# Performance work log

Measured on AMD Instinct MI355X. Metric: run time of the kernel, lower is better.

## Reference

```python
import jax, jax.numpy as jnp
import numpy as np

N_NODES = 50000
N_EDGES = 800000
IN_CH, HID_CH, OUT_CH = 128, 128, 64


def setup_inputs() -> dict:
    key = jax.random.key(0)
    k1, k2, k3, k4, k5, k6 = jax.random.split(key, 6)
    x = jax.random.normal(k1, (N_NODES, IN_CH), dtype=jnp.float32)
    edge_index = jax.random.randint(k2, (2, N_EDGES), 0, N_NODES, dtype=jnp.int64)
    # Glorot init like PyG GCNConv; bias zeros-like but random small for test coverage
    s1 = jnp.sqrt(6.0 / (IN_CH + HID_CH)).astype(jnp.float32)
    s2 = jnp.sqrt(6.0 / (HID_CH + OUT_CH)).astype(jnp.float32)
    W1 = jax.random.uniform(k3, (IN_CH, HID_CH), jnp.float32, -s1, s1)
    b1 = jax.random.normal(k4, (HID_CH,), jnp.float32) * 0.01
    W2 = jax.random.uniform(k5, (HID_CH, OUT_CH), jnp.float32, -s2, s2)
    b2 = jax.random.normal(k6, (OUT_CH,), jnp.float32) * 0.01
    return {"x": x, "edge_index": edge_index, "W1": W1, "b1": b1, "W2": W2, "b2": b2}


def gcn_conv(x, edge_index, W, b):
    """PyG GCNConv: add self-loops, symmetric D^-1/2 (A+I) D^-1/2 normalization,
    then aggregate linearly-transformed neighbor features + bias."""
    n = x.shape[0]
    h = x @ W  # [N, F_out]
    src, dst = edge_index[0], edge_index[1]
    # degree counts self-loop (weight 1) plus in-edges at dst
    deg = 1.0 + jax.ops.segment_sum(jnp.ones_like(src, dtype=h.dtype), dst, num_segments=n)
    dinv = jax.lax.rsqrt(deg)  # deg >= 1, no zeros
    norm = dinv[src] * dinv[dst]  # [E]
    agg = jax.ops.segment_sum(h[src] * norm[:, None], dst, num_segments=n)
    # self-loop contribution: norm = dinv[i]*dinv[i] = 1/deg[i]
    return agg + h * (1.0 / deg)[:, None] + b


def reference(x, edge_index, W1, b1, W2, b2):
    # eval-mode forward: dropout is identity
    h = gcn_conv(x, edge_index, W1, b1)
    h = jax.nn.relu(h)
    out = gcn_conv(h, edge_index, W2, b2)
    return out
```

## Files before the change

### kernel.cpp

```cpp
#include <hip/hip_runtime.h>
#include <hip/hip_fp16.h>


typedef _Float16 f16;
typedef __attribute__((ext_vector_type(8))) _Float16 f16x8;
typedef __attribute__((ext_vector_type(4))) float f32x4;

__global__ __launch_bounds__(256) void deg_prep_kernel(const int* __restrict__ dst,
                                                       int* __restrict__ deg,
                                                       int* __restrict__ posw,
                                                       const float* __restrict__ W1,
                                                       const float* __restrict__ W2,
                                                       f16* __restrict__ Wt1,
                                                       f16* __restrict__ Wt2, int E) {
    int gid = blockIdx.x * 256 + threadIdx.x;
    if (gid < E) posw[gid] = atomicAdd(&deg[dst[gid]], 1);
    if (gid < 128 * 128) {
        int k = gid >> 7, c = gid & 127;
        Wt1[c * 136 + k] = (f16)W1[gid];
    } else if (gid < 128 * 128 + 128 * 64) {
        int j = gid - 128 * 128;
        int k = j >> 6, c = j & 63;
        Wt2[c * 136 + k] = (f16)W2[j];
    }
}

__global__ __launch_bounds__(1024) void scan1_kernel(const int* __restrict__ deg,
                                                     int* __restrict__ rowptr,
                                                     int* __restrict__ bsum,
                                                     float* __restrict__ dinv, int N) {
    __shared__ int wsum[16];
    const int tid = threadIdx.x, lane = tid & 63, wid = tid >> 6;
    const int idx = blockIdx.x * 1024 + tid;
    int v = (idx < N) ? deg[idx] : 0;
    if (idx < N) dinv[idx] = rsqrtf((float)v + 1.0f);
    int incl = v;
#pragma unroll
    for (int off = 1; off < 64; off <<= 1) {
        int t = __shfl_up(incl, off, 64);
        if (lane >= off) incl += t;
    }
    if (lane == 63) wsum[wid] = incl;
    __syncthreads();
    if (wid == 0) {
        int s = (lane < 16) ? wsum[lane] : 0;
#pragma unroll
        for (int off = 1; off < 16; off <<= 1) {
            int t = __shfl_up(s, off, 64);
            if (lane >= off) s += t;
        }
        if (lane < 16) wsum[lane] = s;
    }
    __syncthreads();
    int waveoff = (wid == 0) ? 0 : wsum[wid - 1];
    if (idx < N) rowptr[idx] = waveoff + incl - v;
    if (tid == 1023) bsum[blockIdx.x] = waveoff + incl;
}

__global__ __launch_bounds__(1024) void scan23_kernel(int* __restrict__ rowptr,
                                                      const int* __restrict__ bsum,
                                                      int N, int nb) {
    __shared__ int pfx_s;
    const int tid = threadIdx.x;
    if (tid < 64) {
        int v = (tid < nb && tid < blockIdx.x) ? bsum[tid] : 0;
#pragma unroll
        for (int off = 32; off; off >>= 1) v += __shfl_xor(v, off, 64);
        if (tid == 0) pfx_s = v;
    }
    if (blockIdx.x == 0 && tid >= 64 && tid < 128) {
        int l = tid - 64;
        int v = (l < nb) ? bsum[l] : 0;
#pragma unroll
        for (int off = 32; off; off >>= 1) v += __shfl_xor(v, off, 64);
        if (l == 0) rowptr[N] = v;
    }
    __syncthreads();
    int idx = blockIdx.x * 1024 + tid;
    if (idx < N) rowptr[idx] += pfx_s;
}

__global__ __launch_bounds__(256) void fill_kernel(const int* __restrict__ src,
                                                   const int* __restrict__ dst,
                                                   const int* __restrict__ posw,
                                                   const float* __restrict__ dinv,
                                                   const int* __restrict__ rowptr,
                                                   float2* __restrict__ pairs, int E) {
    int e = blockIdx.x * 256 + threadIdx.x;
    if (e >= E) return;
    int s = src[e], d = dst[e];
    float2 p;
    p.x = __int_as_float(s);
    p.y = dinv[s] * dinv[d];
    pairs[rowptr[d] + posw[e]] = p;
}

template <int KOUT, bool F32IN>
__global__ __launch_bounds__(256) void gemm_kernel(const void* __restrict__ Xv,
                                                   const f16* __restrict__ Wt,
                                                   f16* __restrict__ H, int N) {
    constexpr int CT = KOUT / 16;
    __shared__ f16 Wl[KOUT * 136];
    const int tid = threadIdx.x;
    constexpr int CHUNKS = KOUT * 136 / 8;
    {
        const uint4* s = (const uint4*)Wt;
        uint4* d = (uint4*)Wl;
        for (int i = tid; i < CHUNKS; i += 256) d[i] = s[i];
    }
    __syncthreads();

    const int lane = tid & 63, wid = tid >> 6;
    const int c = lane & 15, kseg = lane >> 4;
    const int row0 = blockIdx.x * 64 + wid * 16;
    int arow = row0 + c;
    if (arow >= N) arow = N - 1;

    f32x4 acc[CT];
#pragma unroll
    for (int t = 0; t < CT; ++t) acc[t] = (f32x4){0.f, 0.f, 0.f, 0.f};

#pragma unroll
    for (int kt = 0; kt < 4; ++kt) {
        const int k0 = kt * 32;
        f16x8 a;
        if (F32IN) {
            const float* xp = (const float*)Xv + (long)arow * 128 + k0 + kseg * 8;
            float4 x0 = *(const float4*)xp;
            float4 x1 = *(const float4*)(xp + 4);
            a[0] = (f16)x0.x; a[1] = (f16)x0.y; a[2] = (f16)x0.z; a[3] = (f16)x0.w;
            a[4] = (f16)x1.x; a[5] = (f16)x1.y; a[6] = (f16)x1.z; a[7] = (f16)x1.w;
        } else {
            a = *(const f16x8*)((const f16*)Xv + (long)arow * 128 + k0 + kseg * 8);
        }
#pragma unroll
        for (int ct = 0; ct < CT; ++ct) {
            f16x8 b = *(const f16x8*)&Wl[(ct * 16 + c) * 136 + k0 + kseg * 8];
            acc[ct] = __builtin_amdgcn_mfma_f32_16x16x32_f16(a, b, acc[ct], 0, 0, 0);
        }
    }

    const int rbase = row0 + kseg * 4;
#pragma unroll
    for (int ct = 0; ct < CT; ++ct)
#pragma unroll
        for (int r = 0; r < 4; ++r) {
            int row = rbase + r;
            if (row < N) H[(long)row * KOUT + ct * 16 + c] = (f16)acc[ct][r];
        }
}

template <int F, bool RELU, bool OUTF16>
__global__ __launch_bounds__(256) void gather_kernel(const void* __restrict__ Hv,
                                                     const int* __restrict__ rowptr,
                                                     const float2* __restrict__ pairs,
                                                     const float* __restrict__ dinv,
                                                     const float* __restrict__ bias,
                                                     void* __restrict__ outv, int N) {
    const int wid = threadIdx.x >> 6;
    const int lane = threadIdx.x & 63;
    const int node = blockIdx.x * 4 + wid;
    if (node >= N) return;
    const int start = rowptr[node], end = rowptr[node + 1];

    if (F == 128) {
        const __half2* Hu = (const __half2*)Hv;
        float ax = 0.f, ay = 0.f;
        int e = start;
        for (; e + 7 < end; e += 8) {
            float2 pp[8];
            __half2 uu[8];
#pragma unroll
            for (int j = 0; j < 8; ++j) pp[j] = pairs[e + j];
#pragma unroll
            for (int j = 0; j < 8; ++j) uu[j] = Hu[(long)__float_as_int(pp[j].x) * 64 + lane];
#pragma unroll
            for (int j = 0; j < 8; ++j) {
                float2 f = __half22float2(uu[j]);
                ax += f.x * pp[j].y;
                ay += f.y * pp[j].y;
            }
        }
        for (; e + 3 < end; e += 4) {
            float2 pp[4];
            __half2 uu[4];
#pragma unroll
            for (int j = 0; j < 4; ++j) pp[j] = pairs[e + j];
#pragma unroll
            for (int j = 0; j < 4; ++j) uu[j] = Hu[(long)__float_as_int(pp[j].x) * 64 + lane];
#pragma unroll
            for (int j = 0; j < 4; ++j) {
                float2 f = __half22float2(uu[j]);
                ax += f.x * pp[j].y;
                ay += f.y * pp[j].y;
            }
        }
        for (; e < end; ++e) {
            float2 p0 = pairs[e];
            float2 f0 = __half22float2(Hu[(long)__float_as_int(p0.x) * 64 + lane]);
            ax += f0.x * p0.y;
            ay += f0.y * p0.y;
        }
        float di = dinv[node];
        float d2 = di * di;
        float2 fs = __half22float2(Hu[(long)node * 64 + lane]);
        float2 bz = ((const float2*)bias)[lane];
        float zx = ax + fs.x * d2 + bz.x;
        float zy = ay + fs.y * d2 + bz.y;
        if (RELU) { zx = fmaxf(zx, 0.f); zy = fmaxf(zy, 0.f); }
        if (OUTF16) {
            ((__half2*)outv)[(long)node * 64 + lane] = __float22half2_rn(make_float2(zx, zy));
        } else {
            float2 o = {zx, zy};
            ((float2*)outv)[(long)node * 64 + lane] = o;
        }
    } else {
        const __half* Hh = (const __half*)Hv;
        float acc = 0.f;
        int e = start;
        for (; e + 7 < end; e += 8) {
            float2 pp[8];
            __half uu[8];
#pragma unroll
            for (int j = 0; j < 8; ++j) pp[j] = pairs[e + j];
#pragma unroll
            for (int j = 0; j < 8; ++j) uu[j] = Hh[(long)__float_as_int(pp[j].x) * 64 + lane];
#pragma unroll
            for (int j = 0; j < 8; ++j) acc += __half2float(uu[j]) * pp[j].y;
        }
        for (; e + 3 < end; e += 4) {
            float2 pp[4];
            __half uu[4];
#pragma unroll
            for (int j = 0; j < 4; ++j) pp[j] = pairs[e + j];
#pragma unroll
            for (int j = 0; j < 4; ++j) uu[j] = Hh[(long)__float_as_int(pp[j].x) * 64 + lane];
#pragma unroll
            for (int j = 0; j < 4; ++j) acc += __half2float(uu[j]) * pp[j].y;
        }
        for (; e < end; ++e) {
            float2 p0 = pairs[e];
            acc += __half2float(Hh[(long)__float_as_int(p0.x) * 64 + lane]) * p0.y;
        }
        float di = dinv[node];
        float z = acc + __half2float(Hh[(long)node * 64 + lane]) * (di * di) + bias[lane];
        if (RELU) z = fmaxf(z, 0.f);
        ((float*)outv)[(long)node * 64 + lane] = z;
    }
}

extern "C" void kernel_launch(void* const* d_in, const int* in_sizes, int n_in,
                              void* d_out, int out_size, void* d_ws, size_t ws_size,
                              hipStream_t stream) {
    const float* x  = (const float*)d_in[0];
    const int*   ei = (const int*)d_in[1];
    const float* W1 = (const float*)d_in[2];
    const float* b1 = (const float*)d_in[3];
    const float* W2 = (const float*)d_in[4];
    const float* b2 = (const float*)d_in[5];
    float* out = (float*)d_out;

    const int N = in_sizes[0] / 128;
    const int E = in_sizes[1] / 2;
    const int* src = ei;
    const int* dst = ei + E;
    const int NB = (N + 1023) / 1024;

    float* ws = (float*)d_ws;
    float2* pairs = (float2*)ws;
    long off = 2L * E;
    int* posw   = (int*)(ws + off); off += E;
    int* deg    = (int*)(ws + off); off += N;
    int* rowptr = (int*)(ws + off); off += N + 1;
    int* bsum   = (int*)(ws + off); off += 64;
    float* dinv = ws + off;        off += N;
    off = (off + 3) & ~3L;
    f16* Wt1 = (f16*)(ws + off); off += (128 * 136) / 2;
    f16* Wt2 = (f16*)(ws + off); off += (64 * 136) / 2;
    f16* h1  = (f16*)(ws + off); off += (long)N * 64;
    f16* z1  = (f16*)(ws + off); off += (long)N * 64;
    f16* h2  = (f16*)(ws + off); off += (long)N * 32;

    hipMemsetAsync(deg, 0, (size_t)N * sizeof(int), stream);
    deg_prep_kernel<<<(E + 255) / 256, 256, 0, stream>>>(dst, deg, posw, W1, W2, Wt1, Wt2, E);
    scan1_kernel<<<NB, 1024, 0, stream>>>(deg, rowptr, bsum, dinv, N);
    scan23_kernel<<<NB, 1024, 0, stream>>>(rowptr, bsum, N, NB);
    fill_kernel<<<(E + 255) / 256, 256, 0, stream>>>(src, dst, posw, dinv, rowptr, pairs, E);

    gemm_kernel<128, true><<<(N + 63) / 64, 256, 0, stream>>>(x, Wt1, h1, N);
    gather_kernel<128, true, true><<<(N + 3) / 4, 256, 0, stream>>>(h1, rowptr, pairs, dinv, b1, z1, N);

    gemm_kernel<64, false><<<(N + 63) / 64, 256, 0, stream>>>(z1, Wt2, h2, N);
    gather_kernel<64, false, false><<<(N + 3) / 4, 256, 0, stream>>>(h2, rowptr, pairs, dinv, b2, out, N);
}
```

Before: 228.2 us.

## Fuse CSR fill with first GEMM and vectorize gather pair loads

Merges the edge-pair fill kernel and the first-layer GEMM into one launch, with block ranges split between the two independent jobs so they run concurrently and one launch is saved. The gather kernels now read the (src, norm) pairs as float4 (two edges per load) after aligning to an even index, and unroll 16 edges per iteration for more outstanding loads. The fill blocks now reserve the 34KB shared array they do not use, which may reduce their occupancy, and the larger unroll raises register pressure.

```diff
diff --git a/kernel.cpp b/kernel.cpp
--- a/kernel.cpp
+++ b/kernel.cpp
@@ -80,27 +80,11 @@
     if (idx < N) rowptr[idx] += pfx_s;
 }
 
-__global__ __launch_bounds__(256) void fill_kernel(const int* __restrict__ src,
-                                                   const int* __restrict__ dst,
-                                                   const int* __restrict__ posw,
-                                                   const float* __restrict__ dinv,
-                                                   const int* __restrict__ rowptr,
-                                                   float2* __restrict__ pairs, int E) {
-    int e = blockIdx.x * 256 + threadIdx.x;
-    if (e >= E) return;
-    int s = src[e], d = dst[e];
-    float2 p;
-    p.x = __int_as_float(s);
-    p.y = dinv[s] * dinv[d];
-    pairs[rowptr[d] + posw[e]] = p;
-}
-
 template <int KOUT, bool F32IN>
-__global__ __launch_bounds__(256) void gemm_kernel(const void* __restrict__ Xv,
-                                                   const f16* __restrict__ Wt,
-                                                   f16* __restrict__ H, int N) {
+__device__ __forceinline__ void gemm_body(int bid, const void* __restrict__ Xv,
+                                          const f16* __restrict__ Wt,
+                                          f16* __restrict__ H, int N, f16* Wl) {
     constexpr int CT = KOUT / 16;
-    __shared__ f16 Wl[KOUT * 136];
     const int tid = threadIdx.x;
     constexpr int CHUNKS = KOUT * 136 / 8;
     {
@@ -112,7 +96,7 @@
 
     const int lane = tid & 63, wid = tid >> 6;
     const int c = lane & 15, kseg = lane >> 4;
-    const int row0 = blockIdx.x * 64 + wid * 16;
+    const int row0 = bid * 64 + wid * 16;
     int arow = row0 + c;
     if (arow >= N) arow = N - 1;
 
@@ -148,6 +132,37 @@
             int row = rbase + r;
             if (row < N) H[(long)row * KOUT + ct * 16 + c] = (f16)acc[ct][r];
         }
+}
+
+template <int KOUT, bool F32IN>
+__global__ __launch_bounds__(256) void gemm_kernel(const void* __restrict__ Xv,
+                                                   const f16* __restrict__ Wt,
+                                                   f16* __restrict__ H, int N) {
+    __shared__ f16 Wl[KOUT * 136];
+    gemm_body<KOUT, F32IN>(blockIdx.x, Xv, Wt, H, N, Wl);
+}
+
+__global__ __launch_bounds__(256) void fill_gemm_kernel(const int* __restrict__ src,
+                                                        const int* __restrict__ dst,
+                                                        const int* __restrict__ posw,
+                                                        const float* __restrict__ dinv,
+                                                        const int* __restrict__ rowptr,
+                                                        float2* __restrict__ pairs, int E,
+                                                        const float* __restrict__ x,
+                                                        const f16* __restrict__ Wt1,
+                                                        f16* __restrict__ h1, int N, int GB) {
+    __shared__ f16 Wl[128 * 136];
+    if ((int)blockIdx.x < GB) {
+        gemm_body<128, true>(blockIdx.x, x, Wt1, h1, N, Wl);
+        return;
+    }
+    int e = (blockIdx.x - GB) * 256 + threadIdx.x;
+    if (e >= E) return;
+    int s = src[e], d = dst[e];
+    float2 p;
+    p.x = __int_as_float(s);
+    p.y = dinv[s] * dinv[d];
+    pairs[rowptr[d] + posw[e]] = p;
 }
 
 template <int F, bool RELU, bool OUTF16>
@@ -162,44 +177,51 @@
     const int node = blockIdx.x * 4 + wid;
     if (node >= N) return;
     const int start = rowptr[node], end = rowptr[node + 1];
+    const float4* pp4 = (const float4*)pairs;
 
     if (F == 128) {
         const __half2* Hu = (const __half2*)Hv;
         float ax = 0.f, ay = 0.f;
         int e = start;
-        for (; e + 7 < end; e += 8) {
-            float2 pp[8];
-            __half2 uu[8];
-#pragma unroll
-            for (int j = 0; j < 8; ++j) pp[j] = pairs[e + j];
-#pragma unroll
-            for (int j = 0; j < 8; ++j) uu[j] = Hu[(long)__float_as_int(pp[j].x) * 64 + lane];
+        if ((e & 1) && e < end) {
+            float2 p0 = pairs[e];
+            float2 f0 = __half22float2(Hu[(long)__float_as_int(p0.x) * 64 + lane]);
+            ax += f0.x * p0.y; ay += f0.y * p0.y;
+            ++e;
+        }
+        for (; e + 15 < end; e += 16) {
+            float4 q[8];
+#pragma unroll
+            for (int j = 0; j < 8; ++j) q[j] = pp4[(e >> 1) + j];
+            __half2 uu[16];
 #pragma unroll
             for (int j = 0; j < 8; ++j) {
-                float2 f = __half22float2(uu[j]);
-                ax += f.x * pp[j].y;
-                ay += f.y * pp[j].y;
+                uu[2 * j]     = Hu[(long)__float_as_int(q[j].x) * 64 + lane];
+                uu[2 * j + 1] = Hu[(long)__float_as_int(q[j].z) * 64 + lane];
             }
+#pragma unroll
+            for (int j = 0; j < 8; ++j) {
+                float2 f0 = __half22float2(uu[2 * j]);
+                float2 f1 = __half22float2(uu[2 * j + 1]);
+                ax += f0.x * q[j].y + f1.x * q[j].w;
+                ay += f0.y * q[j].y + f1.y * q[j].w;
+            }
         }
         for (; e + 3 < end; e += 4) {
-            float2 pp[4];
-            __half2 uu[4];
-#pragma unroll
-            for (int j = 0; j < 4; ++j) pp[j] = pairs[e + j];
-#pragma unroll
-            for (int j = 0; j < 4; ++j) uu[j] = Hu[(long)__float_as_int(pp[j].x) * 64 + lane];
-#pragma unroll
-            for (int j = 0; j < 4; ++j) {
-                float2 f = __half22float2(uu[j]);
-                ax += f.x * pp[j].y;
-                ay += f.y * pp[j].y;
-            }
+            float4 q0 = pp4[e >> 1], q1 = pp4[(e >> 1) + 1];
+            __half2 u0 = Hu[(long)__float_as_int(q0.x) * 64 + lane];
+            __half2 u1 = Hu[(long)__float_as_int(q0.z) * 64 + lane];
+            __half2 u2 = Hu[(long)__float_as_int(q1.x) * 64 + lane];
+            __half2 u3 = Hu[(long)__float_as_int(q1.z) * 64 + lane];
+            float2 f0 = __half22float2(u0), f1 = __half22float2(u1);
+            float2 f2 = __half22float2(u2), f3 = __half22float2(u3);
+            ax += f0.x * q0.y + f1.x * q0.w + f2.x * q1.y + f3.x * q1.w;
+            ay += f0.y * q0.y + f1.y * q0.w + f2.y * q1.y + f3.y * q1.w;
         }
         for (; e < end; ++e) {
             float2 p0 = pairs[e];
             float2 f0 = __half22float2(Hu[(long)__float_as_int(p0.x) * 64 + lane]);
-            ax += f0.x * p0.y;
-            ay += f0.y * p0.y;
+            ax += f0.x * p0.y; ay += f0.y * p0.y;
         }
         float di = dinv[node];
         float d2 = di * di;
@@ -218,25 +240,32 @@
         const __half* Hh = (const __half*)Hv;
         float acc = 0.f;
         int e = start;
-        for (; e + 7 < end; e += 8) {
-            float2 pp[8];
-            __half uu[8];
-#pragma unroll
-            for (int j = 0; j < 8; ++j) pp[j] = pairs[e + j];
-#pragma unroll
-            for (int j = 0; j < 8; ++j) uu[j] = Hh[(long)__float_as_int(pp[j].x) * 64 + lane];
-#pragma unroll
-            for (int j = 0; j < 8; ++j) acc += __half2float(uu[j]) * pp[j].y;
+        if ((e & 1) && e < end) {
+            float2 p0 = pairs[e];
+            acc += __half2float(Hh[(long)__float_as_int(p0.x) * 64 + lane]) * p0.y;
+            ++e;
+        }
+        for (; e + 15 < end; e += 16) {
+            float4 q[8];
+#pragma unroll
+            for (int j = 0; j < 8; ++j) q[j] = pp4[(e >> 1) + j];
+            __half uu[16];
+#pragma unroll
+            for (int j = 0; j < 8; ++j) {
+                uu[2 * j]     = Hh[(long)__float_as_int(q[j].x) * 64 + lane];
+                uu[2 * j + 1] = Hh[(long)__float_as_int(q[j].z) * 64 + lane];
+            }
+#pragma unroll
+            for (int j = 0; j < 8; ++j)
+                acc += __half2float(uu[2 * j]) * q[j].y + __half2float(uu[2 * j + 1]) * q[j].w;
         }
         for (; e + 3 < end; e += 4) {
-            float2 pp[4];
-            __half uu[4];
-#pragma unroll
-            for (int j = 0; j < 4; ++j) pp[j] = pairs[e + j];
-#pragma unroll
-            for (int j = 0; j < 4; ++j) uu[j] = Hh[(long)__float_as_int(pp[j].x) * 64 + lane];
-#pragma unroll
-            for (int j = 0; j < 4; ++j) acc += __half2float(uu[j]) * pp[j].y;
+            float4 q0 = pp4[e >> 1], q1 = pp4[(e >> 1) + 1];
+            float h0 = __half2float(Hh[(long)__float_as_int(q0.x) * 64 + lane]);
+            float h1 = __half2float(Hh[(long)__float_as_int(q0.z) * 64 + lane]);
+            float h2 = __half2float(Hh[(long)__float_as_int(q1.x) * 64 + lane]);
+            float h3 = __half2float(Hh[(long)__float_as_int(q1.z) * 64 + lane]);
+            acc += h0 * q0.y + h1 * q0.w + h2 * q1.y + h3 * q1.w;
         }
         for (; e < end; ++e) {
             float2 p0 = pairs[e];
@@ -285,9 +314,12 @@
     deg_prep_kernel<<<(E + 255) / 256, 256, 0, stream>>>(dst, deg, posw, W1, W2, Wt1, Wt2, E);
     scan1_kernel<<<NB, 1024, 0, stream>>>(deg, rowptr, bsum, dinv, N);
     scan23_kernel<<<NB, 1024, 0, stream>>>(rowptr, bsum, N, NB);
-    fill_kernel<<<(E + 255) / 256, 256, 0, stream>>>(src, dst, posw, dinv, rowptr, pairs, E);
-
-    gemm_kernel<128, true><<<(N + 63) / 64, 256, 0, stream>>>(x, Wt1, h1, N);
+
+    const int GB = (N + 63) / 64;
+    const int FB = (E + 255) / 256;
+    fill_gemm_kernel<<<GB + FB, 256, 0, stream>>>(src, dst, posw, dinv, rowptr, pairs, E,
+                                                  x, Wt1, h1, N, GB);
+
     gather_kernel<128, true, true><<<(N + 3) / 4, 256, 0, stream>>>(h1, rowptr, pairs, dinv, b1, z1, N);
 
     gemm_kernel<64, false><<<(N + 63) / 64, 256, 0, stream>>>(z1, Wt2, h2, N);
```

Result: no change. 228.7 us (+0.2%).
